# Kernel optimization log

Hardware: AMD Instinct MI355X
Metric: run time of the kernel (lower is better)

The kernel has to match this reference:

```python
import jax, jax.numpy as jnp
import numpy as np

N, G, E, D, H = 50000, 1000, 400000, 128, 256


def _sample_negatives(edge_index, batch, rng):
    # Vectorized equivalent of the torch per-edge loop: for each positive edge,
    # draw a dst in the same graph as src, excluding src itself and src's
    # existing neighbors, via 8 rounds of rejection sampling.
    src = edge_index[0]
    counts = np.bincount(batch, minlength=G)
    starts = np.concatenate([[0], np.cumsum(counts)[:-1]])
    g = batch[src]
    edge_keys = np.unique(edge_index[0].astype(np.int64) * N + edge_index[1])
    dst = src.copy()
    valid = np.zeros(E, dtype=bool)
    for _ in range(8):
        cand = starts[g] + rng.integers(0, counts[g])
        ok = (cand != src) & ~np.isin(src.astype(np.int64) * N + cand, edge_keys)
        take = ok & ~valid
        dst = np.where(take, cand, dst)
        valid |= ok
    fallback = starts[g] + (src - starts[g] + 1) % counts[g]  # deterministic in-graph node != src (when graph>1)
    dst = np.where(valid, dst, fallback)
    return np.stack([src, dst]).astype(np.int64)


def setup_inputs() -> dict:
    rng = np.random.default_rng(0)
    batch = np.sort(rng.integers(0, G, size=N)).astype(np.int64)  # contiguous graph ids
    counts = np.bincount(batch, minlength=G)
    starts = np.concatenate([[0], np.cumsum(counts)[:-1]])
    src = rng.integers(0, N, size=E)
    gsrc = batch[src]
    dst = starts[gsrc] + rng.integers(0, counts[gsrc])  # same-graph positive edges
    edge_index = np.stack([src, dst]).astype(np.int64)
    neg_edge_index = _sample_negatives(edge_index, batch, rng)

    key = jax.random.key(0)
    ks = jax.random.split(key, 4)
    x = jax.random.normal(ks[0], (N, D), jnp.float32)
    w1 = jax.random.normal(ks[1], (2 * D, H), jnp.float32) / np.sqrt(2 * D)
    w2 = jax.random.normal(ks[2], (H, H // 2), jnp.float32) / np.sqrt(H)
    w3 = jax.random.normal(ks[3], (H // 2, 1), jnp.float32) / np.sqrt(H // 2)
    return {
        "x": x,
        "edge_index": jnp.asarray(edge_index),
        "batch": jnp.asarray(batch),
        "neg_edge_index": jnp.asarray(neg_edge_index),
        "w1": w1, "b1": jnp.zeros((H,), jnp.float32),
        "g1": jnp.ones((H,), jnp.float32), "be1": jnp.zeros((H,), jnp.float32),
        "w2": w2, "b2": jnp.zeros((H // 2,), jnp.float32),
        "g2": jnp.ones((H // 2,), jnp.float32), "be2": jnp.zeros((H // 2,), jnp.float32),
        "w3": w3, "b3": jnp.zeros((1,), jnp.float32),
    }


def _layernorm(h, g, b, eps=1e-5):
    m = jnp.mean(h, axis=-1, keepdims=True)
    v = jnp.mean(jnp.square(h - m), axis=-1, keepdims=True)
    return (h - m) * jax.lax.rsqrt(v + eps) * g + b


def _edge_mlp(feat, w1, b1, g1, be1, w2, b2, g2, be2, w3, b3):
    h = jax.nn.relu(_layernorm(feat @ w1 + b1, g1, be1))
    h = jax.nn.relu(_layernorm(h @ w2 + b2, g2, be2))
    return jax.nn.sigmoid(h @ w3 + b3)


def reference(x, edge_index, batch, neg_edge_index, w1, b1, g1, be1, w2, b2, g2, be2, w3, b3):
    # batch is consumed by the (setup-time) negative sampler; kept for signature fidelity.
    all_idx = jnp.concatenate([edge_index, neg_edge_index], axis=1)  # [2, 2E]
    feat = jnp.concatenate([x[all_idx[0]], x[all_idx[1]]], axis=-1)  # [2E, 2D]
    pred = _edge_mlp(feat, w1, b1, g1, be1, w2, b2, g2, be2, w3, b3)  # [2E, 1]
    num_pos = edge_index.shape[1]
    num_neg = neg_edge_index.shape[1]
    labels = jnp.concatenate(
        [jnp.ones((num_pos, 1), pred.dtype), jnp.zeros((num_neg, 1), pred.dtype)], axis=0
    )
    return pred, labels
```

## Files before the change

kernel.cpp:

```cpp
#include <hip/hip_runtime.h>
#include <math.h>
#include <stdint.h>

#define NN    50000
#define EPOS  400000
#define ROWS  800000
#define DIM   128
#define D2    256
#define H1C   256
#define H2C   128
#define MT    64
#define NTH   512

typedef __bf16 bf16;
typedef __bf16 bf16x8 __attribute__((ext_vector_type(8)));
typedef __bf16 bf16x4 __attribute__((ext_vector_type(4)));
typedef float  f32x4  __attribute__((ext_vector_type(4)));

#define XB_N   (NN*DIM)
#define W1F_E  XB_N
#define W1F_N  (H1C*D2)
#define W2F_E  (XB_N + W1F_N)
#define W2F_N  (H2C*H1C)
#define WS_NEEDED ((size_t)(XB_N + W1F_N + W2F_N) * 2)

#define AOFF  0
#define SCR   32768
#define SCR2  34816
#define CFOFF 35840
#define SMEM_BYTES 40960

__device__ __forceinline__ void gll16(const void* g, void* l) {
    __builtin_amdgcn_global_load_lds(
        (const __attribute__((address_space(1))) void*)g,
        (__attribute__((address_space(3))) void*)l, 16, 0, 0);
}

__global__ void preconv(const float* __restrict__ x, const float* __restrict__ w1,
                        const float* __restrict__ w2, bf16* __restrict__ ws,
                        float* __restrict__ out) {
    int gi = blockIdx.x * 256 + threadIdx.x;
    if (gi < ROWS) out[ROWS + gi] = (gi < EPOS) ? 1.f : 0.f;
    int i = gi;
    if (i < XB_N) { ws[i] = (bf16)x[i]; return; }
    i -= XB_N;
    if (i < W1F_N) {
        int j = i & 7, l = (i >> 3) & 63, ct = i >> 9;
        int c = ct >> 4, t = ct & 15;
        int n = t * 16 + (l & 15);
        int k = c * 32 + (l >> 4) * 8 + j;
        ws[W1F_E + i] = (bf16)w1[k * H1C + n];
        return;
    }
    i -= W1F_N;
    if (i < W2F_N) {
        int j = i & 7, l = (i >> 3) & 63, ct = i >> 9;
        int c = ct >> 3, t = ct & 7;
        int n = t * 16 + (l & 15);
        int k = c * 32 + (l >> 4) * 8 + j;
        ws[W2F_E + i] = (bf16)w2[k * H2C + n];
    }
}

__global__ __launch_bounds__(NTH, 6) void lp_mfma12(
    const bf16* __restrict__ xb, const bf16* __restrict__ w1f, const bf16* __restrict__ w2f,
    const int*  __restrict__ ei, const int* __restrict__ nei,
    const float* __restrict__ b1, const float* __restrict__ g1, const float* __restrict__ be1,
    const float* __restrict__ b2, const float* __restrict__ g2, const float* __restrict__ be2,
    const float* __restrict__ w3, const float* __restrict__ b3,
    float* __restrict__ out)
{
    extern __shared__ char smem[];
    const int tid  = threadIdx.x;
    const int lane = tid & 63;
    const int w    = tid >> 6;
    const int wm   = w >> 2;
    const int wn   = w & 3;
    const int gr0  = blockIdx.x * MT;
    const int l15  = lane & 15;
    const int l4   = lane >> 4;

    #pragma unroll
    for (int ii = 0; ii < 4; ++ii) {
        const int i = w * 4 + ii;
        uint32_t doff = (uint32_t)(i << 10) + (uint32_t)(lane << 4);
        uint32_t loff = doff ^ (((doff >> 9) & 7u) << 4);
        int row = loff >> 9;
        int inb = loff & 511;
        int gr  = gr0 + row;
        int node;
        if (inb < 256) { node = (gr < EPOS) ? ei[gr]        : nei[gr - EPOS]; }
        else           { node = (gr < EPOS) ? ei[EPOS + gr] : nei[gr]; inb -= 256; }
        gll16((const char*)xb + (((size_t)node) << 8) + inb, smem + AOFF + (i << 10));
    }

    for (int i = tid; i < 1280; i += NTH) {
        float v;
        if      (i < 256)  v = b1[i];
        else if (i < 512)  v = g1[i - 256];
        else if (i < 768)  v = be1[i - 512];
        else if (i < 896)  v = b2[i - 768];
        else if (i < 1024) v = g2[i - 896];
        else if (i < 1152) v = be2[i - 1024];
        else               v = w3[i - 1152];
        *(float*)(smem + CFOFF + i * 4) = v;
    }

    uint32_t abase[2], asw[2];
    #pragma unroll
    for (int mi = 0; mi < 2; ++mi) {
        int row = (wm << 5) + (mi << 4) + l15;
        abase[mi] = (uint32_t)row << 9;
        asw[mi]   = (uint32_t)(row & 7) << 4;
    }
    const uint32_t koff  = (uint32_t)l4 << 4;
    const uint32_t c1off = ((uint32_t)wn << 8) + ((uint32_t)l4 << 4);
    const uint32_t c2off = ((uint32_t)wn << 7) + ((uint32_t)l4 << 4);

    __syncthreads();

    f32x4 acc1s[2][4];
    #pragma unroll
    for (int ni = 0; ni < 4; ++ni) {
        f32x4 bias = *(const f32x4*)(smem + CFOFF + c1off + (ni << 6));
        acc1s[0][ni] = bias; acc1s[1][ni] = bias;
    }
    const bf16* bp1 = w1f + (wn << 11) + (lane << 3);
    #pragma unroll
    for (int c = 0; c < 8; ++c) {
        bf16x8 af[2];
        #pragma unroll
        for (int mi = 0; mi < 2; ++mi)
            af[mi] = *(const bf16x8*)(smem + AOFF + ((abase[mi] + ((uint32_t)c << 6) + koff) ^ asw[mi]));
        #pragma unroll
        for (int ni = 0; ni < 4; ++ni) {
            bf16x8 bfr = *(const bf16x8*)(bp1 + (c << 13) + (ni << 9));
            #pragma unroll
            for (int mi = 0; mi < 2; ++mi)
                acc1s[mi][ni] = __builtin_amdgcn_mfma_f32_16x16x32_bf16(
                    bfr, af[mi], acc1s[mi][ni], 0, 0, 0);
        }
    }

    #pragma unroll
    for (int mi = 0; mi < 2; ++mi) {
        float s1 = 0.f, s2 = 0.f;
        #pragma unroll
        for (int ni = 0; ni < 4; ++ni)
            #pragma unroll
            for (int j = 0; j < 4; ++j) {
                float v = acc1s[mi][ni][j];
                s1 += v; s2 += v * v;
            }
        s1 += __shfl_xor(s1, 16); s1 += __shfl_xor(s1, 32);
        s2 += __shfl_xor(s2, 16); s2 += __shfl_xor(s2, 32);
        if (l4 == 0) {
            int row = (wm << 5) + (mi << 4) + l15;
            *(float2*)(smem + SCR + (row << 5) + (wn << 3)) = make_float2(s1, s2);
        }
    }
    __syncthreads();

    #pragma unroll
    for (int mi = 0; mi < 2; ++mi) {
        int row = (wm << 5) + (mi << 4) + l15;
        f32x4 p0 = *(const f32x4*)(smem + SCR + (row << 5));
        f32x4 p1 = *(const f32x4*)(smem + SCR + (row << 5) + 16);
        float s1 = p0[0] + p0[2] + p1[0] + p1[2];
        float s2 = p0[1] + p0[3] + p1[1] + p1[3];
        float mean = s1 * (1.f / 256.f);
        float var  = s2 * (1.f / 256.f) - mean * mean;
        float rstd = rsqrtf(var + 1e-5f);
        #pragma unroll
        for (int ni = 0; ni < 4; ++ni) {
            f32x4 gv  = *(const f32x4*)(smem + CFOFF + 1024 + c1off + (ni << 6));
            f32x4 bev = *(const f32x4*)(smem + CFOFF + 2048 + c1off + (ni << 6));
            bf16x4 hb;
            #pragma unroll
            for (int j = 0; j < 4; ++j) {
                float h = (acc1s[mi][ni][j] - mean) * rstd * gv[j] + bev[j];
                hb[j] = (bf16)fmaxf(h, 0.f);
            }
            uint32_t byte = ((uint32_t)row << 9) + ((uint32_t)wn << 7) + ((uint32_t)ni << 5) + ((uint32_t)l4 << 3);
            byte ^= ((byte >> 9) & 7u) << 4;
            *(bf16x4*)(smem + AOFF + byte) = hb;
        }
    }
    __syncthreads();

    f32x4 acc2s[2][2];
    #pragma unroll
    for (int ni = 0; ni < 2; ++ni) {
        f32x4 bias = *(const f32x4*)(smem + CFOFF + 3072 + c2off + (ni << 6));
        acc2s[0][ni] = bias; acc2s[1][ni] = bias;
    }
    const bf16* bp2 = w2f + (wn << 10) + (lane << 3);
    #pragma unroll
    for (int c = 0; c < 8; ++c) {
        bf16x8 a2[2];
        #pragma unroll
        for (int mi = 0; mi < 2; ++mi)
            a2[mi] = *(const bf16x8*)(smem + AOFF + ((abase[mi] + ((uint32_t)c << 6) + koff) ^ asw[mi]));
        #pragma unroll
        for (int ni = 0; ni < 2; ++ni) {
            bf16x8 b2r = *(const bf16x8*)(bp2 + (c << 12) + (ni << 9));
            #pragma unroll
            for (int mi = 0; mi < 2; ++mi)
                acc2s[mi][ni] = __builtin_amdgcn_mfma_f32_16x16x32_bf16(
                    b2r, a2[mi], acc2s[mi][ni], 0, 0, 0);
        }
    }

    #pragma unroll
    for (int mi = 0; mi < 2; ++mi) {
        float s1 = 0.f, s2 = 0.f;
        #pragma unroll
        for (int ni = 0; ni < 2; ++ni)
            #pragma unroll
            for (int j = 0; j < 4; ++j) {
                float v = acc2s[mi][ni][j];
                s1 += v; s2 += v * v;
            }
        s1 += __shfl_xor(s1, 16); s1 += __shfl_xor(s1, 32);
        s2 += __shfl_xor(s2, 16); s2 += __shfl_xor(s2, 32);
        if (l4 == 0) {
            int row = (wm << 5) + (mi << 4) + l15;
            *(float2*)(smem + SCR + (row << 5) + (wn << 3)) = make_float2(s1, s2);
        }
    }
    __syncthreads();

    #pragma unroll
    for (int mi = 0; mi < 2; ++mi) {
        int row = (wm << 5) + (mi << 4) + l15;
        f32x4 p0 = *(const f32x4*)(smem + SCR + (row << 5));
        f32x4 p1 = *(const f32x4*)(smem + SCR + (row << 5) + 16);
        float s1 = p0[0] + p0[2] + p1[0] + p1[2];
        float s2 = p0[1] + p0[3] + p1[1] + p1[3];
        float mean = s1 * (1.f / 128.f);
        float var  = s2 * (1.f / 128.f) - mean * mean;
        float rstd = rsqrtf(var + 1e-5f);
        float zp = 0.f;
        #pragma unroll
        for (int ni = 0; ni < 2; ++ni) {
            f32x4 gv  = *(const f32x4*)(smem + CFOFF + 3584 + c2off + (ni << 6));
            f32x4 bev = *(const f32x4*)(smem + CFOFF + 4096 + c2off + (ni << 6));
            f32x4 wv  = *(const f32x4*)(smem + CFOFF + 4608 + c2off + (ni << 6));
            #pragma unroll
            for (int j = 0; j < 4; ++j) {
                float h = (acc2s[mi][ni][j] - mean) * rstd * gv[j] + bev[j];
                h = fmaxf(h, 0.f);
                zp += h * wv[j];
            }
        }
        zp += __shfl_xor(zp, 16); zp += __shfl_xor(zp, 32);
        if (l4 == 0)
            *(float*)(smem + SCR2 + (row << 4) + (wn << 2)) = zp;
    }
    __syncthreads();

    if (wn == 0) {
        const float b3s = b3[0];
        #pragma unroll
        for (int mi = 0; mi < 2; ++mi) {
            int row = (wm << 5) + (mi << 4) + l15;
            if (l4 == 0) {
                f32x4 zv = *(const f32x4*)(smem + SCR2 + (row << 4));
                float z = zv[0] + zv[1] + zv[2] + zv[3] + b3s;
                out[gr0 + row] = 1.f / (1.f + expf(-z));
            }
        }
    }
}

#define TILE  32
#define PAD   264
__global__ __launch_bounds__(256, 4) void lp_fused(
    const float* __restrict__ x, const int* __restrict__ ei, const int* __restrict__ nei,
    const float* __restrict__ w1, const float* __restrict__ b1,
    const float* __restrict__ g1, const float* __restrict__ be1,
    const float* __restrict__ w2, const float* __restrict__ b2,
    const float* __restrict__ g2, const float* __restrict__ be2,
    const float* __restrict__ w3, const float* __restrict__ b3,
    float* __restrict__ out)
{
    __shared__ float lds[TILE][PAD];
    const int t = threadIdx.x, e = t >> 3, jg = t & 7;
    const int row = blockIdx.x * TILE + e;
    {
        int src, dst;
        if (row < EPOS) { src = ei[row];         dst = ei[EPOS + row]; }
        else            { src = nei[row - EPOS]; dst = nei[row]; }
        const float* base = (jg < 4) ? (x + src * DIM + jg * 32) : (x + dst * DIM + (jg - 4) * 32);
        const float4* b4 = (const float4*)base;
        #pragma unroll
        for (int s = 0; s < 8; ++s) *(float4*)&lds[e][jg * 32 + s * 4] = b4[s];
    }
    __syncthreads();
    float acc[32];
    #pragma unroll
    for (int i = 0; i < 32; ++i) acc[i] = 0.f;
    const int j0 = jg * 32;
    for (int k4 = 0; k4 < D2 / 4; ++k4) {
        float4 a4 = *(const float4*)&lds[e][k4 * 4];
        float av[4] = {a4.x, a4.y, a4.z, a4.w};
        #pragma unroll
        for (int kk = 0; kk < 4; ++kk) {
            const float a = av[kk];
            const float4* wr = (const float4*)(w1 + (k4 * 4 + kk) * H1C + j0);
            #pragma unroll
            for (int ii = 0; ii < 8; ++ii) {
                float4 wv = wr[ii];
                acc[ii*4+0] += a*wv.x; acc[ii*4+1] += a*wv.y; acc[ii*4+2] += a*wv.z; acc[ii*4+3] += a*wv.w;
            }
        }
    }
    float s1 = 0.f, s2 = 0.f;
    #pragma unroll
    for (int i = 0; i < 32; ++i) { float h = acc[i] + b1[j0+i]; acc[i] = h; s1 += h; s2 += h*h; }
    #pragma unroll
    for (int m = 1; m < 8; m <<= 1) { s1 += __shfl_xor(s1, m, 8); s2 += __shfl_xor(s2, m, 8); }
    float mean = s1 * (1.f/256.f), var = s2 * (1.f/256.f) - mean*mean, rstd = rsqrtf(var + 1e-5f);
    __syncthreads();
    #pragma unroll
    for (int i = 0; i < 32; ++i)
        lds[e][j0+i] = fmaxf((acc[i]-mean)*rstd*g1[j0+i]+be1[j0+i], 0.f);
    __syncthreads();
    float acc2[16];
    #pragma unroll
    for (int i = 0; i < 16; ++i) acc2[i] = 0.f;
    const int q0 = jg * 16;
    for (int k4 = 0; k4 < H1C / 4; ++k4) {
        float4 a4 = *(const float4*)&lds[e][k4 * 4];
        float av[4] = {a4.x, a4.y, a4.z, a4.w};
        #pragma unroll
        for (int kk = 0; kk < 4; ++kk) {
            const float a = av[kk];
            const float4* wr = (const float4*)(w2 + (k4 * 4 + kk) * H2C + q0);
            #pragma unroll
            for (int ii = 0; ii < 4; ++ii) {
                float4 wv = wr[ii];
                acc2[ii*4+0] += a*wv.x; acc2[ii*4+1] += a*wv.y; acc2[ii*4+2] += a*wv.z; acc2[ii*4+3] += a*wv.w;
            }
        }
    }
    s1 = 0.f; s2 = 0.f;
    #pragma unroll
    for (int i = 0; i < 16; ++i) { float h = acc2[i] + b2[q0+i]; acc2[i] = h; s1 += h; s2 += h*h; }
    #pragma unroll
    for (int m = 1; m < 8; m <<= 1) { s1 += __shfl_xor(s1, m, 8); s2 += __shfl_xor(s2, m, 8); }
    mean = s1 * (1.f/128.f); var = s2 * (1.f/128.f) - mean*mean; rstd = rsqrtf(var + 1e-5f);
    float zp = 0.f;
    #pragma unroll
    for (int i = 0; i < 16; ++i) {
        float h = fmaxf((acc2[i]-mean)*rstd*g2[q0+i]+be2[q0+i], 0.f);
        zp += h * w3[q0+i];
    }
    #pragma unroll
    for (int m = 1; m < 8; m <<= 1) zp += __shfl_xor(zp, m, 8);
    if (jg == 0) out[row] = 1.f / (1.f + expf(-(zp + b3[0])));
    if (jg == 1) out[ROWS + row] = (row < EPOS) ? 1.f : 0.f;
}

extern "C" void kernel_launch(void* const* d_in, const int* in_sizes, int n_in,
                              void* d_out, int out_size, void* d_ws, size_t ws_size,
                              hipStream_t stream) {
    const float* x   = (const float*)d_in[0];
    const int*   ei  = (const int*)d_in[1];
    const int*   nei = (const int*)d_in[3];
    const float* w1  = (const float*)d_in[4];
    const float* b1  = (const float*)d_in[5];
    const float* g1  = (const float*)d_in[6];
    const float* be1 = (const float*)d_in[7];
    const float* w2  = (const float*)d_in[8];
    const float* b2  = (const float*)d_in[9];
    const float* g2  = (const float*)d_in[10];
    const float* be2 = (const float*)d_in[11];
    const float* w3  = (const float*)d_in[12];
    const float* b3  = (const float*)d_in[13];
    float* out = (float*)d_out;

    if (ws_size >= WS_NEEDED) {
        bf16* ws = (bf16*)d_ws;
        const int total = XB_N + W1F_N + W2F_N;
        hipLaunchKernelGGL(preconv, dim3((total + 255) / 256), dim3(256), 0, stream,
                           x, w1, w2, ws, out);
        hipFuncSetAttribute((const void*)lp_mfma12,
                            hipFuncAttributeMaxDynamicSharedMemorySize, SMEM_BYTES);
        hipLaunchKernelGGL(lp_mfma12, dim3(ROWS / MT), dim3(NTH), SMEM_BYTES, stream,
                           ws, ws + W1F_E, ws + W2F_E, ei, nei,
                           b1, g1, be1, b2, g2, be2, w3, b3, out);
    } else {
        hipLaunchKernelGGL(lp_fused, dim3(ROWS / TILE), dim3(256), 0, stream,
                           x, ei, nei, w1, b1, g1, be1, w2, b2, g2, be2, w3, b3, out);
    }
}
```

Measured before the change: 272.7 us.

## Precompute gather byte offsets in preconv and rebalance LayerNorm reductions

The preconversion kernel now also writes a table of 32-bit byte offsets (node<<8) for the source and destination of every row. The main MFMA kernel reads these with a single load per lane instead of branching between the positive and negative edge index arrays. The LayerNorm sum and sum-of-squares and the final dot product are rewritten as tree and FMA reductions to shorten dependency chains. Launch bounds drop from 6 to 4 waves-per-EU, which gives more registers but may lower occupancy, and preconv now does extra work writing 6.4 MB of offsets.

```diff
diff --git a/kernel.cpp b/kernel.cpp
--- a/kernel.cpp
+++ b/kernel.cpp
@@ -20,9 +20,10 @@
 #define XB_N   (NN*DIM)
 #define W1F_E  XB_N
 #define W1F_N  (H1C*D2)
-#define W2F_E  (XB_N + W1F_N)
+#define W2F_E  (W1F_E + W1F_N)
 #define W2F_N  (H2C*H1C)
-#define WS_NEEDED ((size_t)(XB_N + W1F_N + W2F_N) * 2)
+#define OFFS_E (W2F_E + W2F_N)
+#define WS_NEEDED ((size_t)OFFS_E * 2 + (size_t)2 * ROWS * 4)
 
 #define AOFF  0
 #define SCR   32768
@@ -36,9 +37,10 @@
         (__attribute__((address_space(3))) void*)l, 16, 0, 0);
 }
 
-__global__ void preconv(const float* __restrict__ x, const float* __restrict__ w1,
-                        const float* __restrict__ w2, bf16* __restrict__ ws,
-                        float* __restrict__ out) {
+__global__ void preconv3(const float* __restrict__ x, const float* __restrict__ w1,
+                         const float* __restrict__ w2,
+                         const int* __restrict__ ei, const int* __restrict__ nei,
+                         bf16* __restrict__ ws, float* __restrict__ out) {
     int gi = blockIdx.x * 256 + threadIdx.x;
     if (gi < ROWS) out[ROWS + gi] = (gi < EPOS) ? 1.f : 0.f;
     int i = gi;
@@ -59,12 +61,21 @@
         int n = t * 16 + (l & 15);
         int k = c * 32 + (l >> 4) * 8 + j;
         ws[W2F_E + i] = (bf16)w2[k * H2C + n];
+        return;
+    }
+    i -= W2F_N;
+    if (i < 2 * ROWS) {
+        uint32_t* offs = (uint32_t*)(ws + OFFS_E);
+        int node;
+        if (i < ROWS) node = (i < EPOS) ? ei[i] : nei[i - EPOS];
+        else { int gr = i - ROWS; node = (gr < EPOS) ? ei[EPOS + gr] : nei[gr]; }
+        offs[i] = (uint32_t)node << 8;
     }
 }
 
-__global__ __launch_bounds__(NTH, 6) void lp_mfma12(
+__global__ __launch_bounds__(NTH, 4) void lp_mfma13(
     const bf16* __restrict__ xb, const bf16* __restrict__ w1f, const bf16* __restrict__ w2f,
-    const int*  __restrict__ ei, const int* __restrict__ nei,
+    const uint32_t* __restrict__ offs,
     const float* __restrict__ b1, const float* __restrict__ g1, const float* __restrict__ be1,
     const float* __restrict__ b2, const float* __restrict__ g2, const float* __restrict__ be2,
     const float* __restrict__ w3, const float* __restrict__ b3,
@@ -87,11 +98,9 @@
         uint32_t loff = doff ^ (((doff >> 9) & 7u) << 4);
         int row = loff >> 9;
         int inb = loff & 511;
-        int gr  = gr0 + row;
-        int node;
-        if (inb < 256) { node = (gr < EPOS) ? ei[gr]        : nei[gr - EPOS]; }
-        else           { node = (gr < EPOS) ? ei[EPOS + gr] : nei[gr]; inb -= 256; }
-        gll16((const char*)xb + (((size_t)node) << 8) + inb, smem + AOFF + (i << 10));
+        int idx = gr0 + row + ((inb >> 8) ? ROWS : 0);
+        uint32_t off = offs[idx];
+        gll16((const char*)xb + off + (inb & 255), smem + AOFF + (i << 10));
     }
 
     for (int i = tid; i < 1280; i += NTH) {
@@ -144,14 +153,21 @@
 
     #pragma unroll
     for (int mi = 0; mi < 2; ++mi) {
-        float s1 = 0.f, s2 = 0.f;
-        #pragma unroll
-        for (int ni = 0; ni < 4; ++ni)
-            #pragma unroll
-            for (int j = 0; j < 4; ++j) {
-                float v = acc1s[mi][ni][j];
-                s1 += v; s2 += v * v;
-            }
+        f32x4 t01 = acc1s[mi][0] + acc1s[mi][1];
+        f32x4 t23 = acc1s[mi][2] + acc1s[mi][3];
+        f32x4 ts  = t01 + t23;
+        float s1 = (ts[0] + ts[1]) + (ts[2] + ts[3]);
+        float q[4];
+        #pragma unroll
+        for (int ni = 0; ni < 4; ++ni) {
+            f32x4 a = acc1s[mi][ni];
+            float m = a[3] * a[3];
+            m = fmaf(a[2], a[2], m);
+            m = fmaf(a[1], a[1], m);
+            m = fmaf(a[0], a[0], m);
+            q[ni] = m;
+        }
+        float s2 = (q[0] + q[1]) + (q[2] + q[3]);
         s1 += __shfl_xor(s1, 16); s1 += __shfl_xor(s1, 32);
         s2 += __shfl_xor(s2, 16); s2 += __shfl_xor(s2, 32);
         if (l4 == 0) {
@@ -166,8 +182,8 @@
         int row = (wm << 5) + (mi << 4) + l15;
         f32x4 p0 = *(const f32x4*)(smem + SCR + (row << 5));
         f32x4 p1 = *(const f32x4*)(smem + SCR + (row << 5) + 16);
-        float s1 = p0[0] + p0[2] + p1[0] + p1[2];
-        float s2 = p0[1] + p0[3] + p1[1] + p1[3];
+        float s1 = (p0[0] + p0[2]) + (p1[0] + p1[2]);
+        float s2 = (p0[1] + p0[3]) + (p1[1] + p1[3]);
         float mean = s1 * (1.f / 256.f);
         float var  = s2 * (1.f / 256.f) - mean * mean;
         float rstd = rsqrtf(var + 1e-5f);
@@ -213,14 +229,19 @@
 
     #pragma unroll
     for (int mi = 0; mi < 2; ++mi) {
-        float s1 = 0.f, s2 = 0.f;
-        #pragma unroll
-        for (int ni = 0; ni < 2; ++ni)
-            #pragma unroll
-            for (int j = 0; j < 4; ++j) {
-                float v = acc2s[mi][ni][j];
-                s1 += v; s2 += v * v;
-            }
+        f32x4 ts = acc2s[mi][0] + acc2s[mi][1];
+        float s1 = (ts[0] + ts[1]) + (ts[2] + ts[3]);
+        float q[2];
+        #pragma unroll
+        for (int ni = 0; ni < 2; ++ni) {
+            f32x4 a = acc2s[mi][ni];
+            float m = a[3] * a[3];
+            m = fmaf(a[2], a[2], m);
+            m = fmaf(a[1], a[1], m);
+            m = fmaf(a[0], a[0], m);
+            q[ni] = m;
+        }
+        float s2 = q[0] + q[1];
         s1 += __shfl_xor(s1, 16); s1 += __shfl_xor(s1, 32);
         s2 += __shfl_xor(s2, 16); s2 += __shfl_xor(s2, 32);
         if (l4 == 0) {
@@ -235,24 +256,28 @@
         int row = (wm << 5) + (mi << 4) + l15;
         f32x4 p0 = *(const f32x4*)(smem + SCR + (row << 5));
         f32x4 p1 = *(const f32x4*)(smem + SCR + (row << 5) + 16);
-        float s1 = p0[0] + p0[2] + p1[0] + p1[2];
-        float s2 = p0[1] + p0[3] + p1[1] + p1[3];
+        float s1 = (p0[0] + p0[2]) + (p1[0] + p1[2]);
+        float s2 = (p0[1] + p0[3]) + (p1[1] + p1[3]);
         float mean = s1 * (1.f / 128.f);
         float var  = s2 * (1.f / 128.f) - mean * mean;
         float rstd = rsqrtf(var + 1e-5f);
-        float zp = 0.f;
+        float r[2];
         #pragma unroll
         for (int ni = 0; ni < 2; ++ni) {
             f32x4 gv  = *(const f32x4*)(smem + CFOFF + 3584 + c2off + (ni << 6));
             f32x4 bev = *(const f32x4*)(smem + CFOFF + 4096 + c2off + (ni << 6));
             f32x4 wv  = *(const f32x4*)(smem + CFOFF + 4608 + c2off + (ni << 6));
-            #pragma unroll
-            for (int j = 0; j < 4; ++j) {
-                float h = (acc2s[mi][ni][j] - mean) * rstd * gv[j] + bev[j];
-                h = fmaxf(h, 0.f);
-                zp += h * wv[j];
-            }
-        }
+            float h0 = fmaxf((acc2s[mi][ni][0] - mean) * rstd * gv[0] + bev[0], 0.f);
+            float h1 = fmaxf((acc2s[mi][ni][1] - mean) * rstd * gv[1] + bev[1], 0.f);
+            float h2 = fmaxf((acc2s[mi][ni][2] - mean) * rstd * gv[2] + bev[2], 0.f);
+            float h3 = fmaxf((acc2s[mi][ni][3] - mean) * rstd * gv[3] + bev[3], 0.f);
+            float m = h3 * wv[3];
+            m = fmaf(h2, wv[2], m);
+            m = fmaf(h1, wv[1], m);
+            m = fmaf(h0, wv[0], m);
+            r[ni] = m;
+        }
+        float zp = r[0] + r[1];
         zp += __shfl_xor(zp, 16); zp += __shfl_xor(zp, 32);
         if (l4 == 0)
             *(float*)(smem + SCR2 + (row << 4) + (wn << 2)) = zp;
@@ -266,7 +291,7 @@
             int row = (wm << 5) + (mi << 4) + l15;
             if (l4 == 0) {
                 f32x4 zv = *(const f32x4*)(smem + SCR2 + (row << 4));
-                float z = zv[0] + zv[1] + zv[2] + zv[3] + b3s;
+                float z = (zv[0] + zv[1]) + (zv[2] + zv[3]) + b3s;
                 out[gr0 + row] = 1.f / (1.f + expf(-z));
             }
         }
@@ -382,13 +407,14 @@
 
     if (ws_size >= WS_NEEDED) {
         bf16* ws = (bf16*)d_ws;
-        const int total = XB_N + W1F_N + W2F_N;
-        hipLaunchKernelGGL(preconv, dim3((total + 255) / 256), dim3(256), 0, stream,
-                           x, w1, w2, ws, out);
-        hipFuncSetAttribute((const void*)lp_mfma12,
+        const int total = XB_N + W1F_N + W2F_N + 2 * ROWS;
+        hipLaunchKernelGGL(preconv3, dim3((total + 255) / 256), dim3(256), 0, stream,
+                           x, w1, w2, ei, nei, ws, out);
+        hipFuncSetAttribute((const void*)lp_mfma13,
                             hipFuncAttributeMaxDynamicSharedMemorySize, SMEM_BYTES);
-        hipLaunchKernelGGL(lp_mfma12, dim3(ROWS / MT), dim3(NTH), SMEM_BYTES, stream,
-                           ws, ws + W1F_E, ws + W2F_E, ei, nei,
+        hipLaunchKernelGGL(lp_mfma13, dim3(ROWS / MT), dim3(NTH), SMEM_BYTES, stream,
+                           ws, ws + W1F_E, ws + W2F_E,
+                           (const uint32_t*)(ws + OFFS_E),
                            b1, g1, be1, b2, g2, be2, w3, b3, out);
     } else {
         hipLaunchKernelGGL(lp_fused, dim3(ROWS / TILE), dim3(256), 0, stream,
```

After: 248.3 us, median of 2. 1.1x faster.
